# Kernel tuning notes

Measured on AMD Instinct MI355X. Metric: run time of the kernel, lower is better.

Reference implementation:

```python
import jax, jax.numpy as jnp
import numpy as np

# ---- CRF hyperparameters (init_kwargs) ----
NUM_CLASSES = 4
RADIUS = 10            # guided filter radius -> 21x21 kernel
EPS = 1e-4
THETA_GAMMA = 2.5
G_RADIUS = int(THETA_GAMMA * 4)  # gaussian layer radius = 10 -> 21x21 kernel
SPATIAL_COMPAT = 3.0
BILATERAL_COMPAT = 10.0
NUM_ITERATIONS = 5
RGB_W = np.array([0.2989, 0.5870, 0.1140], dtype=np.float32)  # tf rgb_to_grayscale


def _make_kernel(radius, theta):
    x, y = np.mgrid[-radius:radius + 1, -radius:radius + 1]
    k = np.exp(-(x ** 2 + y ** 2) / (2.0 * theta ** 2))
    k = k / k.sum()
    k[radius, radius] = 0.0  # zero out center (no self-message)
    return jnp.asarray(k, dtype=jnp.float32)

_GAUSS_K = _make_kernel(G_RADIUS, THETA_GAMMA)          # spatial gaussian kernel
_GUIDED_K = _make_kernel(RADIUS, RADIUS / 3.0)          # guided-filter gaussian kernel


def _depthwise(src, k2d, r):
    # src: [B,H,W,C], k2d: [kh,kw]; zero-padded depthwise conv (same as pad+VALID)
    c = src.shape[-1]
    kh, kw = k2d.shape
    k = jnp.broadcast_to(k2d[:, :, None, None], (kh, kw, 1, c))
    return jax.lax.conv_general_dilated(
        src, k, window_strides=(1, 1), padding=[(r, r), (r, r)],
        dimension_numbers=('NHWC', 'HWIO', 'NHWC'), feature_group_count=c)


def _gaussian(src):
    return _depthwise(src, _GAUSS_K, G_RADIUS)


def _guided(gray, p):
    # guided gaussian filter with single-channel guide `gray` [B,H,W,1]
    gf = lambda s: _depthwise(s, _GUIDED_K, RADIUS)
    mean_I = gf(gray)                       # [B,H,W,1]
    mean_p = gf(p)                          # [B,H,W,C]
    mean_Ip = gf(gray * p)
    cov_Ip = mean_Ip - mean_I * mean_p
    mean_II = gf(gray * gray)
    var_I = mean_II - mean_I * mean_I
    a = cov_Ip / (var_I + EPS)
    b = mean_p - a * mean_I
    return gf(a) * gray + gf(b)


def setup_inputs() -> dict:
    key = jax.random.key(0)
    k1, k2 = jax.random.split(key)
    unary = jax.random.normal(k1, (1, 512, 512, NUM_CLASSES), dtype=jnp.float32)
    image = jax.random.uniform(k2, (1, 512, 512, 3), dtype=jnp.float32)
    return {"unary": unary, "image": image}


def reference(unary, image):
    gray = (image @ jnp.asarray(RGB_W))[..., None]        # [B,H,W,1]
    ones = jnp.ones_like(unary)
    spatial_norm = _gaussian(ones)
    bilateral_norm = _guided(gray, ones)

    Q = jax.nn.softmax(-unary, axis=-1)
    for _ in range(NUM_ITERATIONS):
        spatial_out = _gaussian(Q) / spatial_norm
        bilateral_out = _guided(gray, Q) / bilateral_norm
        # spatial_weights = SPATIAL_COMPAT*I, bilateral_weights = BILATERAL_COMPAT*I,
        # compatibility = -I  => matmuls reduce to scalar scaling + negation
        message = SPATIAL_COMPAT * spatial_out + BILATERAL_COMPAT * bilateral_out
        pairwise = -message
        Q = jax.nn.softmax(-unary - pairwise, axis=-1)
    return Q
```

## Files before the change

kernel.cpp:

```cpp
#include <hip/hip_runtime.h>
#include <math.h>

#define W 512
#define H 512
#define NPIX (W*H)
#define RAD 10
#define KS 21
#define CRF_EPS 1e-4f

#define TX 32
#define TY 8
#define CIN (TX + 2*RAD)
#define RIN (TY + 2*RAD)
#define GX (W / TX)
#define GY (H / TY)
#define NBLK (GX*GY)
#define NVT (CIN * 4)

#define SM_BYTES 29952
#define OFF_R1 23296

#define FLAG_STRIDE 32

struct W21 { float w[KS]; };

struct Params {
    const float4* unary;
    const float*  image;
    float*  gray;
    float4* Q;
    float2* a1b1;
    float4* a_arr;
    float4* b_arr;
    float4* Qfinal;
    unsigned* flags;
    W21 wg, wu;
    float c0g, c0u;
};

__device__ __forceinline__ float4 f4(float x, float y, float z, float w_) {
    return make_float4(x, y, z, w_);
}
__device__ __forceinline__ float4 fma4(float s, float4 a, float4 acc) {
    acc.x = fmaf(s, a.x, acc.x); acc.y = fmaf(s, a.y, acc.y);
    acc.z = fmaf(s, a.z, acc.z); acc.w = fmaf(s, a.w, acc.w);
    return acc;
}
__device__ __forceinline__ int swz(int b, int N) {
    return (b & 7) * (N >> 3) + (b >> 3);
}


__device__ __forceinline__ void publish(unsigned* flags, int L, unsigned v) {
    __syncthreads();
    if (threadIdx.x == 0)
        __hip_atomic_store(flags + (size_t)L * FLAG_STRIDE, v,
                           __ATOMIC_RELEASE, __HIP_MEMORY_SCOPE_AGENT);
}

__device__ __forceinline__ void waitnb(unsigned* flags, int bx, int by, unsigned v) {
    int t = threadIdx.x;
    if (t < 15) {
        int dx = (t % 3) - 1, dy = (t / 3) - 2;
        int nx = bx + dx, ny = by + dy;
        if (((dx | dy) != 0) && (unsigned)nx < GX && (unsigned)ny < GY) {
            unsigned* f = flags + (size_t)(ny * GX + nx) * FLAG_STRIDE;
            while (__hip_atomic_load(f, __ATOMIC_ACQUIRE,
                                     __HIP_MEMORY_SCOPE_AGENT) < v)
                __builtin_amdgcn_s_sleep(4);
        }
    }
    __syncthreads();
}


__global__ __launch_bounds__(256, 5) void k_crf(Params P) {
    __shared__ __align__(16) char smem[SM_BYTES];
    float4* sQ  = (float4*)smem;
    float2* s2t = (float2*)smem;
    float2* ii0 = (float2*)smem;
    float*  sG  = (float*)(smem + OFF_R1);
    float2* ii1 = (float2*)(smem + OFF_R1);
    float4* i0  = (float4*)smem;
    float4* i1  = (float4*)(smem + 6656);
    float4* i2  = (float4*)(smem + OFF_R1);
    float4* ia  = (float4*)(smem + OFF_R1);
    float4* ib  = (float4*)smem;

    int t = threadIdx.x;
    int L = swz(blockIdx.x, NBLK);
    int bx = L & (GX - 1), by = L >> 4;
    int x0 = bx * TX, y0 = by * TY;
    int row = t >> 5, col = t & 31;
    int py = y0 + row, px = x0 + col;
    int p = py * W + px;
    int vc = t % CIN, vr0 = (t / CIN) * 2;
    int cidx = (row + RAD) * CIN + col + RAD;
    unsigned* flags = P.flags;

    float4 u = P.unary[p];
    {
        float r = P.image[3 * p], g = P.image[3 * p + 1], b = P.image[3 * p + 2];
        P.gray[p] = 0.2989f * r + 0.5870f * g + 0.1140f * b;
        float mn = fminf(fminf(u.x, u.y), fminf(u.z, u.w));
        float ex = expf(mn - u.x), ey = expf(mn - u.y);
        float ez = expf(mn - u.z), ew = expf(mn - u.w);
        float inv = 1.f / (ex + ey + ez + ew);
        P.Q[p] = f4(ex * inv, ey * inv, ez * inv, ew * inv);
    }
    float Sgx = 0.f, Sgy = 0.f, Sux = 0.f, Suy = 0.f;
    #pragma unroll
    for (int d = -RAD; d <= RAD; ++d) {
        int xx = px + d, yy = py + d;
        if (xx >= 0 && xx < W) { Sgx += P.wg.w[d + RAD]; Sux += P.wu.w[d + RAD]; }
        if (yy >= 0 && yy < H) { Sgy += P.wg.w[d + RAD]; Suy += P.wu.w[d + RAD]; }
    }
    float s3 = 3.f / (Sgx * Sgy - P.c0g);
    publish(flags, L, 1);
    waitnb(flags, bx, by, 1);

    for (int i = t; i < RIN * CIN; i += 256) {
        int r = i / CIN, c = i - r * CIN;
        int gx = x0 + c - RAD, gy = y0 + r - RAD;
        float g = 0.f;
        if ((unsigned)gx < W && (unsigned)gy < H) g = P.gray[gy * W + gx];
        sG[i] = g;
    }
    __syncthreads();
    if (t < NVT) {
        float2 acc0 = make_float2(0.f, 0.f), acc1 = acc0;
        #pragma unroll
        for (int s = 0; s < 22; ++s) {
            float g = sG[(vr0 + s) * CIN + vc];
            if (s <= 20) { float wgv = P.wu.w[s] * g; acc0.x += wgv; acc0.y = fmaf(wgv, g, acc0.y); }
            if (s >= 1)  { float wgv = P.wu.w[s-1] * g; acc1.x += wgv; acc1.y = fmaf(wgv, g, acc1.y); }
        }
        ii0[vr0 * CIN + vc] = acc0;
        ii0[(vr0 + 1) * CIN + vc] = acc1;
    }
    __syncthreads();
    float gv = sG[cidx];
    float mI, iv, ibn;
    {
        float2 A = make_float2(0.f, 0.f);
        #pragma unroll
        for (int d = 0; d < KS; ++d) {
            float2 v = ii0[row * CIN + col + d];
            A.x = fmaf(P.wu.w[d], v.x, A.x);
            A.y = fmaf(P.wu.w[d], v.y, A.y);
        }
        mI = A.x - P.c0u * gv;
        float mII = A.y - P.c0u * gv * gv;
        iv = 1.f / ((mII - mI * mI) + CRF_EPS);
        float N = Sux * Suy - P.c0u;
        float a1v = mI * (1.f - N) * iv;
        float b1v = N - a1v * mI;
        P.a1b1[p] = make_float2(a1v, b1v);
    }
    publish(flags, L, 2);
    waitnb(flags, bx, by, 2);

    for (int i = t; i < RIN * CIN; i += 256) {
        int r = i / CIN, c = i - r * CIN;
        int gx = x0 + c - RAD, gy = y0 + r - RAD;
        float2 v = make_float2(0.f, 0.f);
        if ((unsigned)gx < W && (unsigned)gy < H) v = P.a1b1[gy * W + gx];
        s2t[i] = v;
    }
    __syncthreads();
    if (t < NVT) {
        float2 acc0 = make_float2(0.f, 0.f), acc1 = acc0;
        #pragma unroll
        for (int s = 0; s < 22; ++s) {
            float2 v = s2t[(vr0 + s) * CIN + vc];
            if (s <= 20) { acc0.x = fmaf(P.wu.w[s], v.x, acc0.x); acc0.y = fmaf(P.wu.w[s], v.y, acc0.y); }
            if (s >= 1)  { acc1.x = fmaf(P.wu.w[s-1], v.x, acc1.x); acc1.y = fmaf(P.wu.w[s-1], v.y, acc1.y); }
        }
        ii1[vr0 * CIN + vc] = acc0;
        ii1[(vr0 + 1) * CIN + vc] = acc1;
    }
    __syncthreads();
    {
        float2 A = make_float2(0.f, 0.f);
        #pragma unroll
        for (int d = 0; d < KS; ++d) {
            float2 v = ii1[row * CIN + col + d];
            A.x = fmaf(P.wu.w[d], v.x, A.x);
            A.y = fmaf(P.wu.w[d], v.y, A.y);
        }
        float2 cen = s2t[cidx];
        float va = A.x - P.c0u * cen.x;
        float vb = A.y - P.c0u * cen.y;
        ibn = 10.f / (va * gv + vb);
    }

    float px_part, py_part, pz_part, pw_part;
    for (int it = 0; it < 5; ++it) {
        if (it > 0) waitnb(flags, bx, by, 2 + 2 * it);
        __syncthreads();
        for (int i = t; i < RIN * CIN; i += 256) {
            int r = i / CIN, c = i - r * CIN;
            int gx = x0 + c - RAD, gy = y0 + r - RAD;
            float4 q = f4(0.f, 0.f, 0.f, 0.f); float g = 0.f;
            if ((unsigned)gx < W && (unsigned)gy < H) {
                int pp = gy * W + gx; q = P.Q[pp]; g = P.gray[pp];
            }
            sQ[i] = q; sG[i] = g;
        }
        __syncthreads();
        float4 Qc = sQ[cidx];
        float4 a0[2], a1r[2], a2[2];
        if (t < NVT) {
            #pragma unroll
            for (int j = 0; j < 2; ++j) { a0[j] = f4(0,0,0,0); a1r[j] = a0[j]; a2[j] = a0[j]; }
            #pragma unroll
            for (int s = 0; s < 22; ++s) {
                float4 q = sQ[(vr0 + s) * CIN + vc];
                float g = sG[(vr0 + s) * CIN + vc];
                float4 gq = f4(g * q.x, g * q.y, g * q.z, g * q.w);
                if (s <= 20) {
                    a0[0]  = fma4(P.wg.w[s], q, a0[0]);
                    a1r[0] = fma4(P.wu.w[s], q, a1r[0]);
                    a2[0]  = fma4(P.wu.w[s], gq, a2[0]);
                }
                if (s >= 1) {
                    a0[1]  = fma4(P.wg.w[s-1], q, a0[1]);
                    a1r[1] = fma4(P.wu.w[s-1], q, a1r[1]);
                    a2[1]  = fma4(P.wu.w[s-1], gq, a2[1]);
                }
            }
        }
        __syncthreads();
        if (t < NVT) {
            #pragma unroll
            for (int j = 0; j < 2; ++j) {
                i0[(vr0 + j) * CIN + vc] = a0[j];
                i1[(vr0 + j) * CIN + vc] = a1r[j];
                i2[(vr0 + j) * CIN + vc] = a2[j];
            }
        }
        __syncthreads();
        {
            float4 A0 = f4(0,0,0,0), A1 = A0, A2 = A0;
            #pragma unroll
            for (int d = 0; d < KS; ++d) {
                A0 = fma4(P.wg.w[d], i0[row * CIN + col + d], A0);
                A1 = fma4(P.wu.w[d], i1[row * CIN + col + d], A1);
                A2 = fma4(P.wu.w[d], i2[row * CIN + col + d], A2);
            }
            float4 g4  = fma4(-P.c0g, Qc, A0);
            float4 m4  = fma4(-P.c0u, Qc, A1);
            float4 mi4 = fma4(-P.c0u * gv, Qc, A2);
            float4 a, b;
            a.x = (mi4.x - mI * m4.x) * iv; a.y = (mi4.y - mI * m4.y) * iv;
            a.z = (mi4.z - mI * m4.z) * iv; a.w = (mi4.w - mI * m4.w) * iv;
            b.x = m4.x - a.x * mI; b.y = m4.y - a.y * mI;
            b.z = m4.z - a.z * mI; b.w = m4.w - a.w * mI;
            px_part = fmaf(s3, g4.x, -u.x); py_part = fmaf(s3, g4.y, -u.y);
            pz_part = fmaf(s3, g4.z, -u.z); pw_part = fmaf(s3, g4.w, -u.w);
            P.a_arr[p] = a; P.b_arr[p] = b;
        }
        publish(flags, L, 3 + 2 * it);
        waitnb(flags, bx, by, 3 + 2 * it);

        for (int i = t; i < RIN * CIN; i += 256) {
            int r = i / CIN, c = i - r * CIN;
            int gx = x0 + c - RAD, gy = y0 + r - RAD;
            float4 v = f4(0.f, 0.f, 0.f, 0.f);
            if ((unsigned)gx < W && (unsigned)gy < H) v = P.a_arr[gy * W + gx];
            sQ[i] = v;
        }
        __syncthreads();
        float4 Ac = sQ[cidx];
        if (t < NVT) {
            float4 va0 = f4(0,0,0,0), va1 = va0;
            #pragma unroll
            for (int s = 0; s < 22; ++s) {
                float4 v = sQ[(vr0 + s) * CIN + vc];
                if (s <= 20) va0 = fma4(P.wu.w[s], v, va0);
                if (s >= 1)  va1 = fma4(P.wu.w[s-1], v, va1);
            }
            ia[vr0 * CIN + vc] = va0;
            ia[(vr0 + 1) * CIN + vc] = va1;
        }
        __syncthreads();
        for (int i = t; i < RIN * CIN; i += 256) {
            int r = i / CIN, c = i - r * CIN;
            int gx = x0 + c - RAD, gy = y0 + r - RAD;
            float4 v = f4(0.f, 0.f, 0.f, 0.f);
            if ((unsigned)gx < W && (unsigned)gy < H) v = P.b_arr[gy * W + gx];
            sQ[i] = v;
        }
        __syncthreads();
        float4 Bc = sQ[cidx];
        float4 vb0 = f4(0,0,0,0), vb1 = vb0;
        if (t < NVT) {
            #pragma unroll
            for (int s = 0; s < 22; ++s) {
                float4 v = sQ[(vr0 + s) * CIN + vc];
                if (s <= 20) vb0 = fma4(P.wu.w[s], v, vb0);
                if (s >= 1)  vb1 = fma4(P.wu.w[s-1], v, vb1);
            }
        }
        __syncthreads();
        if (t < NVT) {
            ib[vr0 * CIN + vc] = vb0;
            ib[(vr0 + 1) * CIN + vc] = vb1;
        }
        __syncthreads();
        {
            float4 VA = f4(0,0,0,0), VB = VA;
            #pragma unroll
            for (int d = 0; d < KS; ++d) {
                VA = fma4(P.wu.w[d], ia[row * CIN + col + d], VA);
                VB = fma4(P.wu.w[d], ib[row * CIN + col + d], VB);
            }
            float4 a4 = fma4(-P.c0u, Ac, VA);
            float4 b4 = fma4(-P.c0u, Bc, VB);
            float lx = fmaf(fmaf(a4.x, gv, b4.x), ibn, px_part);
            float ly = fmaf(fmaf(a4.y, gv, b4.y), ibn, py_part);
            float lz = fmaf(fmaf(a4.z, gv, b4.z), ibn, pz_part);
            float lw = fmaf(fmaf(a4.w, gv, b4.w), ibn, pw_part);
            float m = fmaxf(fmaxf(lx, ly), fmaxf(lz, lw));
            float ex = expf(lx - m), ey = expf(ly - m);
            float ez = expf(lz - m), ew = expf(lw - m);
            float inv = 1.f / (ex + ey + ez + ew);
            float4 qn = f4(ex * inv, ey * inv, ez * inv, ew * inv);
            if (it == 4) P.Qfinal[p] = qn;
            else         P.Q[p] = qn;
        }
        if (it < 4) publish(flags, L, 4 + 2 * it);
    }
}


__global__ __launch_bounds__(256) void fb_init(const float* __restrict__ img,
        const float4* __restrict__ unary, float* __restrict__ gray,
        float4* __restrict__ Q, float* __restrict__ Sg, float* __restrict__ Su,
        W21 wg, W21 wu) {
    int t = threadIdx.x;
    if (blockIdx.x < 2) {
        int x = blockIdx.x * 256 + t;
        float sg = 0.f, su = 0.f;
        #pragma unroll
        for (int d = -RAD; d <= RAD; ++d) {
            int xx = x + d;
            if (xx >= 0 && xx < W) { sg += wg.w[d + RAD]; su += wu.w[d + RAD]; }
        }
        Sg[x] = sg; Su[x] = su;
    }
    int b = swz(blockIdx.x, NPIX / 256);
    int p = b * 256 + t;
    float r = img[3 * p], g = img[3 * p + 1], bch = img[3 * p + 2];
    gray[p] = 0.2989f * r + 0.5870f * g + 0.1140f * bch;
    float4 u = unary[p];
    float mn = fminf(fminf(u.x, u.y), fminf(u.z, u.w));
    float ex = expf(mn - u.x), ey = expf(mn - u.y), ez = expf(mn - u.z), ew = expf(mn - u.w);
    float inv = 1.f / (ex + ey + ez + ew);
    Q[p] = f4(ex * inv, ey * inv, ez * inv, ew * inv);
}

__global__ __launch_bounds__(256, 4) void fb_s1(const float* __restrict__ gray,
        const float* __restrict__ Su, float* __restrict__ mean_I,
        float* __restrict__ inv_var, float2* __restrict__ a1b1,
        W21 wu, float c0u) {
    __shared__ float  sg[RIN][CIN];
    __shared__ float2 ii[TY][CIN];
    int L = swz(blockIdx.x, NBLK);
    int x0 = (L & (GX - 1)) * TX, y0 = (L >> 4) * TY;
    int t = threadIdx.x;
    for (int i = t; i < RIN * CIN; i += 256) {
        int r = i / CIN, c = i - r * CIN;
        int gx = x0 + c - RAD, gy = y0 + r - RAD;
        float g = 0.f;
        if ((unsigned)gx < W && (unsigned)gy < H) g = gray[gy * W + gx];
        sg[r][c] = g;
    }
    __syncthreads();
    if (t < NVT) {
        int c = t % CIN, r0 = (t / CIN) * 2;
        float2 acc0 = make_float2(0.f, 0.f), acc1 = acc0;
        #pragma unroll
        for (int s = 0; s < 22; ++s) {
            float g = sg[r0 + s][c];
            if (s <= 20) { float wgv = wu.w[s] * g; acc0.x += wgv; acc0.y = fmaf(wgv, g, acc0.y); }
            if (s >= 1)  { float wgv = wu.w[s-1] * g; acc1.x += wgv; acc1.y = fmaf(wgv, g, acc1.y); }
        }
        ii[r0][c] = acc0; ii[r0 + 1][c] = acc1;
    }
    __syncthreads();
    int row = t >> 5, col = t & 31;
    float2 A = make_float2(0.f, 0.f);
    #pragma unroll
    for (int d = 0; d < KS; ++d) {
        float2 v = ii[row][col + d];
        A.x = fmaf(wu.w[d], v.x, A.x);
        A.y = fmaf(wu.w[d], v.y, A.y);
    }
    int py = y0 + row, px = x0 + col;
    int p = py * W + px;
    float gc = sg[row + RAD][col + RAD];
    float mI = A.x - c0u * gc;
    float mII = A.y - c0u * gc * gc;
    float iv = 1.f / ((mII - mI * mI) + CRF_EPS);
    float N = Su[px] * Su[py] - c0u;
    float av = mI * (1.f - N) * iv;
    float bv = N - av * mI;
    mean_I[p] = mI; inv_var[p] = iv; a1b1[p] = make_float2(av, bv);
}

__global__ __launch_bounds__(256, 4) void fb_s2(const float2* __restrict__ a1b1,
        const float* __restrict__ gray, float* __restrict__ inv_bn,
        W21 wu, float c0u) {
    __shared__ float2 s2[RIN][CIN];
    __shared__ float2 ii[TY][CIN];
    int L = swz(blockIdx.x, NBLK);
    int x0 = (L & (GX - 1)) * TX, y0 = (L >> 4) * TY;
    int t = threadIdx.x;
    for (int i = t; i < RIN * CIN; i += 256) {
        int r = i / CIN, c = i - r * CIN;
        int gx = x0 + c - RAD, gy = y0 + r - RAD;
        float2 v = make_float2(0.f, 0.f);
        if ((unsigned)gx < W && (unsigned)gy < H) v = a1b1[gy * W + gx];
        s2[r][c] = v;
    }
    __syncthreads();
    if (t < NVT) {
        int c = t % CIN, r0 = (t / CIN) * 2;
        float2 acc0 = make_float2(0.f, 0.f), acc1 = acc0;
        #pragma unroll
        for (int s = 0; s < 22; ++s) {
            float2 v = s2[r0 + s][c];
            if (s <= 20) { acc0.x = fmaf(wu.w[s], v.x, acc0.x); acc0.y = fmaf(wu.w[s], v.y, acc0.y); }
            if (s >= 1)  { acc1.x = fmaf(wu.w[s-1], v.x, acc1.x); acc1.y = fmaf(wu.w[s-1], v.y, acc1.y); }
        }
        ii[r0][c] = acc0; ii[r0 + 1][c] = acc1;
    }
    __syncthreads();
    int row = t >> 5, col = t & 31;
    float2 A = make_float2(0.f, 0.f);
    #pragma unroll
    for (int d = 0; d < KS; ++d) {
        float2 v = ii[row][col + d];
        A.x = fmaf(wu.w[d], v.x, A.x);
        A.y = fmaf(wu.w[d], v.y, A.y);
    }
    int p = (y0 + row) * W + x0 + col;
    float2 cen = s2[row + RAD][col + RAD];
    float va = A.x - c0u * cen.x;
    float vb = A.y - c0u * cen.y;
    inv_bn[p] = 1.f / (va * gray[p] + vb);
}

__global__ __launch_bounds__(256, 4) void fb_f1(const float4* __restrict__ Q,
        const float* __restrict__ gray, const float* __restrict__ mean_I,
        const float* __restrict__ inv_var, const float* __restrict__ Sg,
        const float4* __restrict__ unary, float4* __restrict__ a_out,
        float4* __restrict__ b_out, float4* __restrict__ partial,
        W21 wg, W21 wu, float c0g, float c0u) {
    __shared__ __align__(16) char smem[23296 + 5824 + 6656];
    float4* sQ = (float4*)smem;
    float*  sG = (float*)(smem + 23296);
    float4* i2 = (float4*)(smem + 23296 + 5824);
    float4* i0 = (float4*)smem;
    float4* i1 = (float4*)(smem + 6656);
    int L = swz(blockIdx.x, NBLK);
    int x0 = (L & (GX - 1)) * TX, y0 = (L >> 4) * TY;
    int t = threadIdx.x;
    for (int i = t; i < RIN * CIN; i += 256) {
        int r = i / CIN, c = i - r * CIN;
        int gx = x0 + c - RAD, gy = y0 + r - RAD;
        float4 q = f4(0.f, 0.f, 0.f, 0.f); float g = 0.f;
        if ((unsigned)gx < W && (unsigned)gy < H) {
            int p = gy * W + gx; q = Q[p]; g = gray[p];
        }
        sQ[i] = q; sG[i] = g;
    }
    __syncthreads();
    int row = t >> 5, col = t & 31;
    int py = y0 + row, px = x0 + col;
    int p = py * W + px;
    float mI = mean_I[p], iv = inv_var[p];
    float4 u = unary[p];
    float sgx = Sg[px], sgy = Sg[py];
    float4 Qc = sQ[(row + RAD) * CIN + col + RAD];
    float  gc = sG[(row + RAD) * CIN + col + RAD];
    float4 a0[2], a1[2], a2[2];
    int vc = t % CIN, vr0 = (t / CIN) * 2;
    if (t < NVT) {
        #pragma unroll
        for (int j = 0; j < 2; ++j) { a0[j] = f4(0,0,0,0); a1[j] = a0[j]; a2[j] = a0[j]; }
        #pragma unroll
        for (int s = 0; s < 22; ++s) {
            float4 q = sQ[(vr0 + s) * CIN + vc];
            float g = sG[(vr0 + s) * CIN + vc];
            float4 gq = f4(g * q.x, g * q.y, g * q.z, g * q.w);
            if (s <= 20) {
                a0[0] = fma4(wg.w[s], q, a0[0]);
                a1[0] = fma4(wu.w[s], q, a1[0]);
                a2[0] = fma4(wu.w[s], gq, a2[0]);
            }
            if (s >= 1) {
                a0[1] = fma4(wg.w[s-1], q, a0[1]);
                a1[1] = fma4(wu.w[s-1], q, a1[1]);
                a2[1] = fma4(wu.w[s-1], gq, a2[1]);
            }
        }
    }
    __syncthreads();
    if (t < NVT) {
        #pragma unroll
        for (int j = 0; j < 2; ++j) {
            i0[(vr0 + j) * CIN + vc] = a0[j];
            i1[(vr0 + j) * CIN + vc] = a1[j];
            i2[(vr0 + j) * CIN + vc] = a2[j];
        }
    }
    __syncthreads();
    float4 A0 = f4(0,0,0,0), A1 = A0, A2 = A0;
    #pragma unroll
    for (int d = 0; d < KS; ++d) {
        A0 = fma4(wg.w[d], i0[row * CIN + col + d], A0);
        A1 = fma4(wu.w[d], i1[row * CIN + col + d], A1);
        A2 = fma4(wu.w[d], i2[row * CIN + col + d], A2);
    }
    float4 g4  = fma4(-c0g, Qc, A0);
    float4 m4  = fma4(-c0u, Qc, A1);
    float4 mi4 = fma4(-c0u * gc, Qc, A2);
    float4 a, b;
    a.x = (mi4.x - mI * m4.x) * iv; a.y = (mi4.y - mI * m4.y) * iv;
    a.z = (mi4.z - mI * m4.z) * iv; a.w = (mi4.w - mI * m4.w) * iv;
    b.x = m4.x - a.x * mI; b.y = m4.y - a.y * mI;
    b.z = m4.z - a.z * mI; b.w = m4.w - a.w * mI;
    float s3 = 3.f / (sgx * sgy - c0g);
    float4 part = f4(fmaf(s3, g4.x, -u.x), fmaf(s3, g4.y, -u.y),
                     fmaf(s3, g4.z, -u.z), fmaf(s3, g4.w, -u.w));
    a_out[p] = a; b_out[p] = b; partial[p] = part;
}

__global__ __launch_bounds__(256, 4) void fb_f2(const float4* __restrict__ A,
        const float4* __restrict__ B, const float4* __restrict__ partial,
        const float* __restrict__ gray, const float* __restrict__ inv_bn,
        float4* __restrict__ Qout, W21 wu, float c0u) {
    __shared__ __align__(16) char smem[23296 + 6656];
    float4* sT = (float4*)smem;
    float4* ia = (float4*)(smem + 23296);
    float4* ib = (float4*)smem;
    int L = swz(blockIdx.x, NBLK);
    int x0 = (L & (GX - 1)) * TX, y0 = (L >> 4) * TY;
    int t = threadIdx.x;
    int row = t >> 5, col = t & 31;
    int py = y0 + row, px = x0 + col;
    int p = py * W + px;
    int vc = t % CIN, vr0 = (t / CIN) * 2;
    float gv = gray[p];
    float ibn = 10.f * inv_bn[p];
    float4 part = partial[p];
    for (int i = t; i < RIN * CIN; i += 256) {
        int r = i / CIN, c = i - r * CIN;
        int gx = x0 + c - RAD, gy = y0 + r - RAD;
        float4 v = f4(0.f, 0.f, 0.f, 0.f);
        if ((unsigned)gx < W && (unsigned)gy < H) v = A[gy * W + gx];
        sT[i] = v;
    }
    __syncthreads();
    float4 Ac = sT[(row + RAD) * CIN + col + RAD];
    float4 va0 = f4(0,0,0,0), va1 = va0;
    if (t < NVT) {
        #pragma unroll
        for (int s = 0; s < 22; ++s) {
            float4 v = sT[(vr0 + s) * CIN + vc];
            if (s <= 20) va0 = fma4(wu.w[s], v, va0);
            if (s >= 1)  va1 = fma4(wu.w[s-1], v, va1);
        }
        ia[vr0 * CIN + vc] = va0;
        ia[(vr0 + 1) * CIN + vc] = va1;
    }
    __syncthreads();
    for (int i = t; i < RIN * CIN; i += 256) {
        int r = i / CIN, c = i - r * CIN;
        int gx = x0 + c - RAD, gy = y0 + r - RAD;
        float4 v = f4(0.f, 0.f, 0.f, 0.f);
        if ((unsigned)gx < W && (unsigned)gy < H) v = B[gy * W + gx];
        sT[i] = v;
    }
    __syncthreads();
    float4 Bc = sT[(row + RAD) * CIN + col + RAD];
    float4 vb0 = f4(0,0,0,0), vb1 = vb0;
    if (t < NVT) {
        #pragma unroll
        for (int s = 0; s < 22; ++s) {
            float4 v = sT[(vr0 + s) * CIN + vc];
            if (s <= 20) vb0 = fma4(wu.w[s], v, vb0);
            if (s >= 1)  vb1 = fma4(wu.w[s-1], v, vb1);
        }
    }
    __syncthreads();
    if (t < NVT) {
        ib[vr0 * CIN + vc] = vb0;
        ib[(vr0 + 1) * CIN + vc] = vb1;
    }
    __syncthreads();
    float4 VA = f4(0,0,0,0), VB = VA;
    #pragma unroll
    for (int d = 0; d < KS; ++d) {
        VA = fma4(wu.w[d], ia[row * CIN + col + d], VA);
        VB = fma4(wu.w[d], ib[row * CIN + col + d], VB);
    }
    float4 a4 = fma4(-c0u, Ac, VA);
    float4 b4 = fma4(-c0u, Bc, VB);
    float lx = fmaf(fmaf(a4.x, gv, b4.x), ibn, part.x);
    float ly = fmaf(fmaf(a4.y, gv, b4.y), ibn, part.y);
    float lz = fmaf(fmaf(a4.z, gv, b4.z), ibn, part.z);
    float lw = fmaf(fmaf(a4.w, gv, b4.w), ibn, part.w);
    float m = fmaxf(fmaxf(lx, ly), fmaxf(lz, lw));
    float ex = expf(lx - m), ey = expf(ly - m), ez = expf(lz - m), ew = expf(lw - m);
    float inv = 1.f / (ex + ey + ez + ew);
    Qout[p] = f4(ex * inv, ey * inv, ez * inv, ew * inv);
}


static void make_w_host(double theta, W21* w, float* c0) {
    double tmp[KS], s = 0.0;
    for (int d = -RAD; d <= RAD; ++d) {
        double v = exp(-(double)(d * d) / (2.0 * theta * theta));
        tmp[d + RAD] = v; s += v;
    }
    for (int i = 0; i < KS; ++i) w->w[i] = (float)(tmp[i] / s);
    *c0 = (float)(1.0 / (s * s));
}

extern "C" void kernel_launch(void* const* d_in, const int* in_sizes, int n_in,
                              void* d_out, int out_size, void* d_ws, size_t ws_size,
                              hipStream_t stream) {
    const float4* unary = (const float4*)d_in[0];
    const float* image = (const float*)d_in[1];
    float* wsf = (float*)d_ws;

    float*  gray    = wsf;
    float*  mean_I  = wsf + 262144;
    float*  inv_var = wsf + 524288;
    float2* a1b1    = (float2*)(wsf + 786432);
    float*  inv_bn  = wsf + 1310720;
    float*  Sg      = wsf + 1572864;
    float*  Su      = wsf + 1573376;
    float4* Q       = (float4*)(wsf + 1573888);
    float4* partial = (float4*)(wsf + 2622464);
    float4* a_arr   = (float4*)(wsf + 3671040);
    float4* b_arr   = (float4*)(wsf + 4719616);
    unsigned* flags = (unsigned*)(wsf + 262144);

    W21 wg, wu; float c0g, c0u;
    make_w_host(2.5, &wg, &c0g);
    make_w_host(10.0 / 3.0, &wu, &c0u);

    int dev = 0;
    (void)hipGetDevice(&dev);
    int coop = 0, nCU = 0, blkPerCU = 0;
    (void)hipDeviceGetAttribute(&coop, hipDeviceAttributeCooperativeLaunch, dev);
    (void)hipDeviceGetAttribute(&nCU, hipDeviceAttributeMultiprocessorCount, dev);
    (void)hipOccupancyMaxActiveBlocksPerMultiprocessor(&blkPerCU,
            (const void*)k_crf, 256, 0);
    bool useCoop = (coop != 0) && ((long)blkPerCU * nCU >= NBLK);

    hipError_t st = hipErrorUnknown;
    if (useCoop) {
        (void)hipMemsetAsync(flags, 0, (size_t)NBLK * FLAG_STRIDE * sizeof(unsigned),
                             stream);
        Params P;
        P.unary = unary; P.image = image; P.gray = gray; P.Q = Q;
        P.a1b1 = a1b1; P.a_arr = a_arr; P.b_arr = b_arr;
        P.Qfinal = (float4*)d_out; P.flags = flags;
        P.wg = wg; P.wu = wu; P.c0g = c0g; P.c0u = c0u;
        void* args[] = { &P };
        st = hipLaunchCooperativeKernel((const void*)k_crf, dim3(NBLK), dim3(256),
                                        args, 0, stream);
    }
    if (st != hipSuccess) {
        dim3 bl(256), grEl(NPIX / 256), grT(NBLK);
        fb_init<<<grEl, bl, 0, stream>>>(image, unary, gray, Q, Sg, Su, wg, wu);
        fb_s1<<<grT, bl, 0, stream>>>(gray, Su, mean_I, inv_var, a1b1, wu, c0u);
        fb_s2<<<grT, bl, 0, stream>>>(a1b1, gray, inv_bn, wu, c0u);
        for (int it = 0; it < 5; ++it) {
            fb_f1<<<grT, bl, 0, stream>>>(Q, gray, mean_I, inv_var, Sg,
                                          unary, a_arr, b_arr, partial, wg, wu, c0g, c0u);
            float4* qdst = (it == 4) ? (float4*)d_out : Q;
            fb_f2<<<grT, bl, 0, stream>>>(a_arr, b_arr, partial, gray, inv_bn, qdst,
                                          wu, c0u);
        }
    }
}
```

Before: 170.4 us.

## Register-block separable filters: 4 rows per vertical thread, 2 pixels per horizontal thread

The vertical pass now has each of 104 threads compute 4 output rows from a 24-row sliding window, where before each of 208 threads computed 2 rows from 22. The horizontal pass now has 128 threads each produce 2 adjacent pixels, reading from even/odd split shared-memory planes so each loaded value feeds both outputs. Gray is kept resident in shared memory instead of being reloaded every iteration, which enlarges the LDS footprint and lowers launch bounds from 5 to 4 waves. The aim is fewer redundant LDS reads per FMA. The cost is that only half the threads stay active in the compute phases, register pressure rises, and occupancy drops.

```diff
diff --git a/kernel.cpp b/kernel.cpp
--- a/kernel.cpp
+++ b/kernel.cpp
@@ -17,8 +17,9 @@
 #define NBLK (GX*GY)
 #define NVT (CIN * 4)
 
-#define SM_BYTES 29952
-#define OFF_R1 23296
+#define SM_BYTES 35776
+#define OFF_SG 23296
+#define OFF_R2 29120
 
 #define FLAG_STRIDE 32
 
@@ -50,7 +51,6 @@
     return (b & 7) * (N >> 3) + (b >> 3);
 }
 
-
 __device__ __forceinline__ void publish(unsigned* flags, int L, unsigned v) {
     __syncthreads();
     if (threadIdx.x == 0)
@@ -67,55 +67,70 @@
             unsigned* f = flags + (size_t)(ny * GX + nx) * FLAG_STRIDE;
             while (__hip_atomic_load(f, __ATOMIC_ACQUIRE,
                                      __HIP_MEMORY_SCOPE_AGENT) < v)
-                __builtin_amdgcn_s_sleep(4);
-        }
-    }
-    __syncthreads();
-}
-
-
-__global__ __launch_bounds__(256, 5) void k_crf(Params P) {
+                __builtin_amdgcn_s_sleep(2);
+        }
+    }
+    __syncthreads();
+}
+
+
+__global__ __launch_bounds__(256, 4) void k_crf(Params P) {
     __shared__ __align__(16) char smem[SM_BYTES];
     float4* sQ  = (float4*)smem;
     float2* s2t = (float2*)smem;
-    float2* ii0 = (float2*)smem;
-    float*  sG  = (float*)(smem + OFF_R1);
-    float2* ii1 = (float2*)(smem + OFF_R1);
-    float4* i0  = (float4*)smem;
-    float4* i1  = (float4*)(smem + 6656);
-    float4* i2  = (float4*)(smem + OFF_R1);
-    float4* ia  = (float4*)(smem + OFF_R1);
-    float4* ib  = (float4*)smem;
+    float*  sG  = (float*)(smem + OFF_SG);
+    float4* i0E = (float4*)smem;
+    float4* i1E = (float4*)(smem + 6656);
+    float4* i2E = (float4*)(smem + 13312);
+    float4* iaE = (float4*)(smem + OFF_R2);
+    float4* ibE = (float4*)smem;
+    float2* ii0E = (float2*)smem;
+    float2* ii1E = (float2*)(smem + OFF_R2);
 
     int t = threadIdx.x;
     int L = swz(blockIdx.x, NBLK);
     int bx = L & (GX - 1), by = L >> 4;
     int x0 = bx * TX, y0 = by * TY;
     int row = t >> 5, col = t & 31;
-    int py = y0 + row, px = x0 + col;
-    int p = py * W + px;
-    int vc = t % CIN, vr0 = (t / CIN) * 2;
-    int cidx = (row + RAD) * CIN + col + RAD;
+    int p = (y0 + row) * W + x0 + col;
+    int vc = t % CIN, vr4 = (t / CIN) * 4;
+    int hrow = t >> 4, hm = t & 15;
+    int c0 = 2 * hm;
+    int hpy = y0 + hrow;
+    int p0 = hpy * W + x0 + c0, p1 = p0 + 1;
+    int cidx0 = (hrow + RAD) * CIN + c0 + RAD;
+    int cidx1 = cidx0 + 1;
+    int hb = hrow * 26 + hm;
     unsigned* flags = P.flags;
 
-    float4 u = P.unary[p];
     {
         float r = P.image[3 * p], g = P.image[3 * p + 1], b = P.image[3 * p + 2];
         P.gray[p] = 0.2989f * r + 0.5870f * g + 0.1140f * b;
-        float mn = fminf(fminf(u.x, u.y), fminf(u.z, u.w));
-        float ex = expf(mn - u.x), ey = expf(mn - u.y);
-        float ez = expf(mn - u.z), ew = expf(mn - u.w);
+        float4 uu = P.unary[p];
+        float mn = fminf(fminf(uu.x, uu.y), fminf(uu.z, uu.w));
+        float ex = expf(mn - uu.x), ey = expf(mn - uu.y);
+        float ez = expf(mn - uu.z), ew = expf(mn - uu.w);
         float inv = 1.f / (ex + ey + ez + ew);
         P.Q[p] = f4(ex * inv, ey * inv, ez * inv, ew * inv);
     }
-    float Sgx = 0.f, Sgy = 0.f, Sux = 0.f, Suy = 0.f;
-    #pragma unroll
-    for (int d = -RAD; d <= RAD; ++d) {
-        int xx = px + d, yy = py + d;
-        if (xx >= 0 && xx < W) { Sgx += P.wg.w[d + RAD]; Sux += P.wu.w[d + RAD]; }
-        if (yy >= 0 && yy < H) { Sgy += P.wg.w[d + RAD]; Suy += P.wu.w[d + RAD]; }
-    }
-    float s3 = 3.f / (Sgx * Sgy - P.c0g);
+    float4 u0, u1; float s30, s31, N0, N1;
+    if (t < 128) {
+        u0 = P.unary[p0]; u1 = P.unary[p1];
+        float Sgy = 0.f, Suy = 0.f, Sgx0 = 0.f, Sux0 = 0.f, Sgx1 = 0.f, Sux1 = 0.f;
+        #pragma unroll
+        for (int d = -RAD; d <= RAD; ++d) {
+            int yy = hpy + d;
+            if ((unsigned)yy < H) { Sgy += P.wg.w[d + RAD]; Suy += P.wu.w[d + RAD]; }
+            int xa = x0 + c0 + d;
+            if ((unsigned)xa < W) { Sgx0 += P.wg.w[d + RAD]; Sux0 += P.wu.w[d + RAD]; }
+            int xb = xa + 1;
+            if ((unsigned)xb < W) { Sgx1 += P.wg.w[d + RAD]; Sux1 += P.wu.w[d + RAD]; }
+        }
+        s30 = 3.f / (Sgx0 * Sgy - P.c0g);
+        s31 = 3.f / (Sgx1 * Sgy - P.c0g);
+        N0 = Sux0 * Suy - P.c0u;
+        N1 = Sux1 * Suy - P.c0u;
+    }
     publish(flags, L, 1);
     waitnb(flags, bx, by, 1);
 
@@ -127,35 +142,61 @@
         sG[i] = g;
     }
     __syncthreads();
-    if (t < NVT) {
-        float2 acc0 = make_float2(0.f, 0.f), acc1 = acc0;
-        #pragma unroll
-        for (int s = 0; s < 22; ++s) {
-            float g = sG[(vr0 + s) * CIN + vc];
-            if (s <= 20) { float wgv = P.wu.w[s] * g; acc0.x += wgv; acc0.y = fmaf(wgv, g, acc0.y); }
-            if (s >= 1)  { float wgv = P.wu.w[s-1] * g; acc1.x += wgv; acc1.y = fmaf(wgv, g, acc1.y); }
-        }
-        ii0[vr0 * CIN + vc] = acc0;
-        ii0[(vr0 + 1) * CIN + vc] = acc1;
-    }
-    __syncthreads();
-    float gv = sG[cidx];
-    float mI, iv, ibn;
     {
-        float2 A = make_float2(0.f, 0.f);
-        #pragma unroll
-        for (int d = 0; d < KS; ++d) {
-            float2 v = ii0[row * CIN + col + d];
-            A.x = fmaf(P.wu.w[d], v.x, A.x);
-            A.y = fmaf(P.wu.w[d], v.y, A.y);
-        }
-        mI = A.x - P.c0u * gv;
-        float mII = A.y - P.c0u * gv * gv;
-        iv = 1.f / ((mII - mI * mI) + CRF_EPS);
-        float N = Sux * Suy - P.c0u;
-        float a1v = mI * (1.f - N) * iv;
-        float b1v = N - a1v * mI;
-        P.a1b1[p] = make_float2(a1v, b1v);
+        float2 A[4];
+        if (t < 104) {
+            #pragma unroll
+            for (int j = 0; j < 4; ++j) A[j] = make_float2(0.f, 0.f);
+            #pragma unroll
+            for (int s = 0; s < 24; ++s) {
+                float g = sG[(vr4 + s) * CIN + vc];
+                #pragma unroll
+                for (int j = 0; j < 4; ++j) {
+                    int d = s - j;
+                    if (d >= 0 && d <= 20) {
+                        float wgv = P.wu.w[d] * g;
+                        A[j].x += wgv; A[j].y = fmaf(wgv, g, A[j].y);
+                    }
+                }
+            }
+        }
+        __syncthreads();
+        if (t < 104) {
+            float2* pl = ii0E + (vc & 1) * 208;
+            #pragma unroll
+            for (int j = 0; j < 4; ++j) pl[(vr4 + j) * 26 + (vc >> 1)] = A[j];
+        }
+        __syncthreads();
+    }
+    float gv0 = 0.f, gv1 = 0.f, mI0, mI1, iv0, iv1, ibn0, ibn1;
+    if (t < 128) {
+        gv0 = sG[cidx0]; gv1 = sG[cidx1];
+        float2 a0 = make_float2(0.f, 0.f), a1 = a0;
+        #pragma unroll
+        for (int k = 0; k <= 10; ++k) {
+            float2 e = ii0E[hb + k], o = ii0E[208 + hb + k];
+            float we = P.wu.w[2 * k];
+            a0.x = fmaf(we, e.x, a0.x); a0.y = fmaf(we, e.y, a0.y);
+            a1.x = fmaf(we, o.x, a1.x); a1.y = fmaf(we, o.y, a1.y);
+            if (k < 10) {
+                float wo = P.wu.w[2 * k + 1];
+                a0.x = fmaf(wo, o.x, a0.x); a0.y = fmaf(wo, o.y, a0.y);
+            }
+            if (k > 0) {
+                float wp = P.wu.w[2 * k - 1];
+                a1.x = fmaf(wp, e.x, a1.x); a1.y = fmaf(wp, e.y, a1.y);
+            }
+        }
+        mI0 = a0.x - P.c0u * gv0;
+        float mII0 = a0.y - P.c0u * gv0 * gv0;
+        iv0 = 1.f / ((mII0 - mI0 * mI0) + CRF_EPS);
+        float av0 = mI0 * (1.f - N0) * iv0;
+        P.a1b1[p0] = make_float2(av0, N0 - av0 * mI0);
+        mI1 = a1.x - P.c0u * gv1;
+        float mII1 = a1.y - P.c0u * gv1 * gv1;
+        iv1 = 1.f / ((mII1 - mI1 * mI1) + CRF_EPS);
+        float av1 = mI1 * (1.f - N1) * iv1;
+        P.a1b1[p1] = make_float2(av1, N1 - av1 * mI1);
     }
     publish(flags, L, 2);
     waitnb(flags, bx, by, 2);
@@ -168,97 +209,157 @@
         s2t[i] = v;
     }
     __syncthreads();
-    if (t < NVT) {
-        float2 acc0 = make_float2(0.f, 0.f), acc1 = acc0;
-        #pragma unroll
-        for (int s = 0; s < 22; ++s) {
-            float2 v = s2t[(vr0 + s) * CIN + vc];
-            if (s <= 20) { acc0.x = fmaf(P.wu.w[s], v.x, acc0.x); acc0.y = fmaf(P.wu.w[s], v.y, acc0.y); }
-            if (s >= 1)  { acc1.x = fmaf(P.wu.w[s-1], v.x, acc1.x); acc1.y = fmaf(P.wu.w[s-1], v.y, acc1.y); }
-        }
-        ii1[vr0 * CIN + vc] = acc0;
-        ii1[(vr0 + 1) * CIN + vc] = acc1;
-    }
-    __syncthreads();
     {
-        float2 A = make_float2(0.f, 0.f);
-        #pragma unroll
-        for (int d = 0; d < KS; ++d) {
-            float2 v = ii1[row * CIN + col + d];
-            A.x = fmaf(P.wu.w[d], v.x, A.x);
-            A.y = fmaf(P.wu.w[d], v.y, A.y);
-        }
-        float2 cen = s2t[cidx];
-        float va = A.x - P.c0u * cen.x;
-        float vb = A.y - P.c0u * cen.y;
-        ibn = 10.f / (va * gv + vb);
-    }
-
-    float px_part, py_part, pz_part, pw_part;
+        float2 A[4];
+        if (t < 104) {
+            #pragma unroll
+            for (int j = 0; j < 4; ++j) A[j] = make_float2(0.f, 0.f);
+            #pragma unroll
+            for (int s = 0; s < 24; ++s) {
+                float2 v = s2t[(vr4 + s) * CIN + vc];
+                #pragma unroll
+                for (int j = 0; j < 4; ++j) {
+                    int d = s - j;
+                    if (d >= 0 && d <= 20) {
+                        float w_ = P.wu.w[d];
+                        A[j].x = fmaf(w_, v.x, A[j].x);
+                        A[j].y = fmaf(w_, v.y, A[j].y);
+                    }
+                }
+            }
+        }
+        __syncthreads();
+        if (t < 104) {
+            float2* pl = ii1E + (vc & 1) * 208;
+            #pragma unroll
+            for (int j = 0; j < 4; ++j) pl[(vr4 + j) * 26 + (vc >> 1)] = A[j];
+        }
+        __syncthreads();
+    }
+    if (t < 128) {
+        float2 a0 = make_float2(0.f, 0.f), a1 = a0;
+        #pragma unroll
+        for (int k = 0; k <= 10; ++k) {
+            float2 e = ii1E[hb + k], o = ii1E[208 + hb + k];
+            float we = P.wu.w[2 * k];
+            a0.x = fmaf(we, e.x, a0.x); a0.y = fmaf(we, e.y, a0.y);
+            a1.x = fmaf(we, o.x, a1.x); a1.y = fmaf(we, o.y, a1.y);
+            if (k < 10) {
+                float wo = P.wu.w[2 * k + 1];
+                a0.x = fmaf(wo, o.x, a0.x); a0.y = fmaf(wo, o.y, a0.y);
+            }
+            if (k > 0) {
+                float wp = P.wu.w[2 * k - 1];
+                a1.x = fmaf(wp, e.x, a1.x); a1.y = fmaf(wp, e.y, a1.y);
+            }
+        }
+        float2 cen0 = s2t[cidx0], cen1 = s2t[cidx1];
+        float va0 = a0.x - P.c0u * cen0.x, vb0 = a0.y - P.c0u * cen0.y;
+        ibn0 = 10.f / (va0 * gv0 + vb0);
+        float va1 = a1.x - P.c0u * cen1.x, vb1 = a1.y - P.c0u * cen1.y;
+        ibn1 = 10.f / (va1 * gv1 + vb1);
+    }
+
+    float4 part0, part1;
     for (int it = 0; it < 5; ++it) {
         if (it > 0) waitnb(flags, bx, by, 2 + 2 * it);
         __syncthreads();
         for (int i = t; i < RIN * CIN; i += 256) {
             int r = i / CIN, c = i - r * CIN;
             int gx = x0 + c - RAD, gy = y0 + r - RAD;
-            float4 q = f4(0.f, 0.f, 0.f, 0.f); float g = 0.f;
-            if ((unsigned)gx < W && (unsigned)gy < H) {
-                int pp = gy * W + gx; q = P.Q[pp]; g = P.gray[pp];
-            }
-            sQ[i] = q; sG[i] = g;
+            float4 q = f4(0.f, 0.f, 0.f, 0.f);
+            if ((unsigned)gx < W && (unsigned)gy < H) q = P.Q[gy * W + gx];
+            sQ[i] = q;
         }
         __syncthreads();
-        float4 Qc = sQ[cidx];
-        float4 a0[2], a1r[2], a2[2];
-        if (t < NVT) {
-            #pragma unroll
-            for (int j = 0; j < 2; ++j) { a0[j] = f4(0,0,0,0); a1r[j] = a0[j]; a2[j] = a0[j]; }
-            #pragma unroll
-            for (int s = 0; s < 22; ++s) {
-                float4 q = sQ[(vr0 + s) * CIN + vc];
-                float g = sG[(vr0 + s) * CIN + vc];
-                float4 gq = f4(g * q.x, g * q.y, g * q.z, g * q.w);
-                if (s <= 20) {
-                    a0[0]  = fma4(P.wg.w[s], q, a0[0]);
-                    a1r[0] = fma4(P.wu.w[s], q, a1r[0]);
-                    a2[0]  = fma4(P.wu.w[s], gq, a2[0]);
-                }
-                if (s >= 1) {
-                    a0[1]  = fma4(P.wg.w[s-1], q, a0[1]);
-                    a1r[1] = fma4(P.wu.w[s-1], q, a1r[1]);
-                    a2[1]  = fma4(P.wu.w[s-1], gq, a2[1]);
-                }
-            }
-        }
-        __syncthreads();
-        if (t < NVT) {
-            #pragma unroll
-            for (int j = 0; j < 2; ++j) {
-                i0[(vr0 + j) * CIN + vc] = a0[j];
-                i1[(vr0 + j) * CIN + vc] = a1r[j];
-                i2[(vr0 + j) * CIN + vc] = a2[j];
-            }
-        }
-        __syncthreads();
+        float4 Qc0, Qc1;
+        if (t < 128) { Qc0 = sQ[cidx0]; Qc1 = sQ[cidx1]; }
         {
-            float4 A0 = f4(0,0,0,0), A1 = A0, A2 = A0;
-            #pragma unroll
-            for (int d = 0; d < KS; ++d) {
-                A0 = fma4(P.wg.w[d], i0[row * CIN + col + d], A0);
-                A1 = fma4(P.wu.w[d], i1[row * CIN + col + d], A1);
-                A2 = fma4(P.wu.w[d], i2[row * CIN + col + d], A2);
-            }
-            float4 g4  = fma4(-P.c0g, Qc, A0);
-            float4 m4  = fma4(-P.c0u, Qc, A1);
-            float4 mi4 = fma4(-P.c0u * gv, Qc, A2);
-            float4 a, b;
-            a.x = (mi4.x - mI * m4.x) * iv; a.y = (mi4.y - mI * m4.y) * iv;
-            a.z = (mi4.z - mI * m4.z) * iv; a.w = (mi4.w - mI * m4.w) * iv;
-            b.x = m4.x - a.x * mI; b.y = m4.y - a.y * mI;
-            b.z = m4.z - a.z * mI; b.w = m4.w - a.w * mI;
-            px_part = fmaf(s3, g4.x, -u.x); py_part = fmaf(s3, g4.y, -u.y);
-            pz_part = fmaf(s3, g4.z, -u.z); pw_part = fmaf(s3, g4.w, -u.w);
-            P.a_arr[p] = a; P.b_arr[p] = b;
+            float4 A0[4], A1[4], A2[4];
+            if (t < 104) {
+                #pragma unroll
+                for (int j = 0; j < 4; ++j) {
+                    A0[j] = f4(0,0,0,0); A1[j] = A0[j]; A2[j] = A0[j];
+                }
+                #pragma unroll
+                for (int s = 0; s < 24; ++s) {
+                    float4 q = sQ[(vr4 + s) * CIN + vc];
+                    float g = sG[(vr4 + s) * CIN + vc];
+                    float4 gq = f4(g * q.x, g * q.y, g * q.z, g * q.w);
+                    #pragma unroll
+                    for (int j = 0; j < 4; ++j) {
+                        int d = s - j;
+                        if (d >= 0 && d <= 20) {
+                            A0[j] = fma4(P.wg.w[d], q, A0[j]);
+                            A1[j] = fma4(P.wu.w[d], q, A1[j]);
+                            A2[j] = fma4(P.wu.w[d], gq, A2[j]);
+                        }
+                    }
+                }
+            }
+            __syncthreads();
+            if (t < 104) {
+                int pb = (vc & 1) * 208, ci = vc >> 1;
+                #pragma unroll
+                for (int j = 0; j < 4; ++j) {
+                    int rw = (vr4 + j) * 26 + ci;
+                    i0E[pb + rw] = A0[j];
+                    i1E[pb + rw] = A1[j];
+                    i2E[pb + rw] = A2[j];
+                }
+            }
+            __syncthreads();
+        }
+        if (t < 128) {
+            float4 G0 = f4(0,0,0,0), G1 = G0, M0 = G0, M1 = G0, X0 = G0, X1 = G0;
+            #pragma unroll
+            for (int k = 0; k <= 10; ++k) {
+                float4 e0 = i0E[hb + k], o0 = i0E[208 + hb + k];
+                float4 e1 = i1E[hb + k], o1 = i1E[208 + hb + k];
+                float4 e2 = i2E[hb + k], o2 = i2E[208 + hb + k];
+                float wge = P.wg.w[2 * k], wue = P.wu.w[2 * k];
+                G0 = fma4(wge, e0, G0);  G1 = fma4(wge, o0, G1);
+                M0 = fma4(wue, e1, M0);  M1 = fma4(wue, o1, M1);
+                X0 = fma4(wue, e2, X0);  X1 = fma4(wue, o2, X1);
+                if (k < 10) {
+                    float wgo = P.wg.w[2 * k + 1], wuo = P.wu.w[2 * k + 1];
+                    G0 = fma4(wgo, o0, G0);
+                    M0 = fma4(wuo, o1, M0);
+                    X0 = fma4(wuo, o2, X0);
+                }
+                if (k > 0) {
+                    float wgp = P.wg.w[2 * k - 1], wup = P.wu.w[2 * k - 1];
+                    G1 = fma4(wgp, e0, G1);
+                    M1 = fma4(wup, e1, M1);
+                    X1 = fma4(wup, e2, X1);
+                }
+            }
+            {
+                float4 g4  = fma4(-P.c0g, Qc0, G0);
+                float4 m4  = fma4(-P.c0u, Qc0, M0);
+                float4 mi4 = fma4(-P.c0u * gv0, Qc0, X0);
+                float4 a, b;
+                a.x = (mi4.x - mI0 * m4.x) * iv0; a.y = (mi4.y - mI0 * m4.y) * iv0;
+                a.z = (mi4.z - mI0 * m4.z) * iv0; a.w = (mi4.w - mI0 * m4.w) * iv0;
+                b.x = m4.x - a.x * mI0; b.y = m4.y - a.y * mI0;
+                b.z = m4.z - a.z * mI0; b.w = m4.w - a.w * mI0;
+                part0 = f4(fmaf(s30, g4.x, -u0.x), fmaf(s30, g4.y, -u0.y),
+                           fmaf(s30, g4.z, -u0.z), fmaf(s30, g4.w, -u0.w));
+                P.a_arr[p0] = a; P.b_arr[p0] = b;
+            }
+            {
+                float4 g4  = fma4(-P.c0g, Qc1, G1);
+                float4 m4  = fma4(-P.c0u, Qc1, M1);
+                float4 mi4 = fma4(-P.c0u * gv1, Qc1, X1);
+                float4 a, b;
+                a.x = (mi4.x - mI1 * m4.x) * iv1; a.y = (mi4.y - mI1 * m4.y) * iv1;
+                a.z = (mi4.z - mI1 * m4.z) * iv1; a.w = (mi4.w - mI1 * m4.w) * iv1;
+                b.x = m4.x - a.x * mI1; b.y = m4.y - a.y * mI1;
+                b.z = m4.z - a.z * mI1; b.w = m4.w - a.w * mI1;
+                part1 = f4(fmaf(s31, g4.x, -u1.x), fmaf(s31, g4.y, -u1.y),
+                           fmaf(s31, g4.z, -u1.z), fmaf(s31, g4.w, -u1.w));
+                P.a_arr[p1] = a; P.b_arr[p1] = b;
+            }
         }
         publish(flags, L, 3 + 2 * it);
         waitnb(flags, bx, by, 3 + 2 * it);
@@ -271,17 +372,24 @@
             sQ[i] = v;
         }
         __syncthreads();
-        float4 Ac = sQ[cidx];
-        if (t < NVT) {
-            float4 va0 = f4(0,0,0,0), va1 = va0;
-            #pragma unroll
-            for (int s = 0; s < 22; ++s) {
-                float4 v = sQ[(vr0 + s) * CIN + vc];
-                if (s <= 20) va0 = fma4(P.wu.w[s], v, va0);
-                if (s >= 1)  va1 = fma4(P.wu.w[s-1], v, va1);
-            }
-            ia[vr0 * CIN + vc] = va0;
-            ia[(vr0 + 1) * CIN + vc] = va1;
+        float4 Ac0, Ac1;
+        if (t < 128) { Ac0 = sQ[cidx0]; Ac1 = sQ[cidx1]; }
+        if (t < 104) {
+            float4 VA[4];
+            #pragma unroll
+            for (int j = 0; j < 4; ++j) VA[j] = f4(0,0,0,0);
+            #pragma unroll
+            for (int s = 0; s < 24; ++s) {
+                float4 v = sQ[(vr4 + s) * CIN + vc];
+                #pragma unroll
+                for (int j = 0; j < 4; ++j) {
+                    int d = s - j;
+                    if (d >= 0 && d <= 20) VA[j] = fma4(P.wu.w[d], v, VA[j]);
+                }
+            }
+            int pb = (vc & 1) * 208, ci = vc >> 1;
+            #pragma unroll
+            for (int j = 0; j < 4; ++j) iaE[pb + (vr4 + j) * 26 + ci] = VA[j];
         }
         __syncthreads();
         for (int i = t; i < RIN * CIN; i += 256) {
@@ -292,42 +400,79 @@
             sQ[i] = v;
         }
         __syncthreads();
-        float4 Bc = sQ[cidx];
-        float4 vb0 = f4(0,0,0,0), vb1 = vb0;
-        if (t < NVT) {
-            #pragma unroll
-            for (int s = 0; s < 22; ++s) {
-                float4 v = sQ[(vr0 + s) * CIN + vc];
-                if (s <= 20) vb0 = fma4(P.wu.w[s], v, vb0);
-                if (s >= 1)  vb1 = fma4(P.wu.w[s-1], v, vb1);
-            }
-        }
-        __syncthreads();
-        if (t < NVT) {
-            ib[vr0 * CIN + vc] = vb0;
-            ib[(vr0 + 1) * CIN + vc] = vb1;
-        }
-        __syncthreads();
+        float4 Bc0, Bc1;
+        if (t < 128) { Bc0 = sQ[cidx0]; Bc1 = sQ[cidx1]; }
         {
-            float4 VA = f4(0,0,0,0), VB = VA;
-            #pragma unroll
-            for (int d = 0; d < KS; ++d) {
-                VA = fma4(P.wu.w[d], ia[row * CIN + col + d], VA);
-                VB = fma4(P.wu.w[d], ib[row * CIN + col + d], VB);
-            }
-            float4 a4 = fma4(-P.c0u, Ac, VA);
-            float4 b4 = fma4(-P.c0u, Bc, VB);
-            float lx = fmaf(fmaf(a4.x, gv, b4.x), ibn, px_part);
-            float ly = fmaf(fmaf(a4.y, gv, b4.y), ibn, py_part);
-            float lz = fmaf(fmaf(a4.z, gv, b4.z), ibn, pz_part);
-            float lw = fmaf(fmaf(a4.w, gv, b4.w), ibn, pw_part);
-            float m = fmaxf(fmaxf(lx, ly), fmaxf(lz, lw));
-            float ex = expf(lx - m), ey = expf(ly - m);
-            float ez = expf(lz - m), ew = expf(lw - m);
-            float inv = 1.f / (ex + ey + ez + ew);
-            float4 qn = f4(ex * inv, ey * inv, ez * inv, ew * inv);
-            if (it == 4) P.Qfinal[p] = qn;
-            else         P.Q[p] = qn;
+            float4 VB[4];
+            if (t < 104) {
+                #pragma unroll
+                for (int j = 0; j < 4; ++j) VB[j] = f4(0,0,0,0);
+                #pragma unroll
+                for (int s = 0; s < 24; ++s) {
+                    float4 v = sQ[(vr4 + s) * CIN + vc];
+                    #pragma unroll
+                    for (int j = 0; j < 4; ++j) {
+                        int d = s - j;
+                        if (d >= 0 && d <= 20) VB[j] = fma4(P.wu.w[d], v, VB[j]);
+                    }
+                }
+            }
+            __syncthreads();
+            if (t < 104) {
+                int pb = (vc & 1) * 208, ci = vc >> 1;
+                #pragma unroll
+                for (int j = 0; j < 4; ++j) ibE[pb + (vr4 + j) * 26 + ci] = VB[j];
+            }
+            __syncthreads();
+        }
+        if (t < 128) {
+            float4 VA0 = f4(0,0,0,0), VA1 = VA0, VB0 = VA0, VB1 = VA0;
+            #pragma unroll
+            for (int k = 0; k <= 10; ++k) {
+                float4 ea = iaE[hb + k], oa = iaE[208 + hb + k];
+                float4 eb = ibE[hb + k], ob = ibE[208 + hb + k];
+                float wue = P.wu.w[2 * k];
+                VA0 = fma4(wue, ea, VA0);  VA1 = fma4(wue, oa, VA1);
+                VB0 = fma4(wue, eb, VB0);  VB1 = fma4(wue, ob, VB1);
+                if (k < 10) {
+                    float wuo = P.wu.w[2 * k + 1];
+                    VA0 = fma4(wuo, oa, VA0);
+                    VB0 = fma4(wuo, ob, VB0);
+                }
+                if (k > 0) {
+                    float wup = P.wu.w[2 * k - 1];
+                    VA1 = fma4(wup, ea, VA1);
+                    VB1 = fma4(wup, eb, VB1);
+                }
+            }
+            {
+                float4 a4 = fma4(-P.c0u, Ac0, VA0);
+                float4 b4 = fma4(-P.c0u, Bc0, VB0);
+                float lx = fmaf(fmaf(a4.x, gv0, b4.x), ibn0, part0.x);
+                float ly = fmaf(fmaf(a4.y, gv0, b4.y), ibn0, part0.y);
+                float lz = fmaf(fmaf(a4.z, gv0, b4.z), ibn0, part0.z);
+                float lw = fmaf(fmaf(a4.w, gv0, b4.w), ibn0, part0.w);
+                float m = fmaxf(fmaxf(lx, ly), fmaxf(lz, lw));
+                float ex = expf(lx - m), ey = expf(ly - m);
+                float ez = expf(lz - m), ew = expf(lw - m);
+                float inv = 1.f / (ex + ey + ez + ew);
+                float4 qn = f4(ex * inv, ey * inv, ez * inv, ew * inv);
+                if (it == 4) P.Qfinal[p0] = qn; else P.Q[p0] = qn;
+            }
+            {
+                float4 a4 = fma4(-P.c0u, Ac1, VA1);
+                float4 b4 = fma4(-P.c0u, Bc1, VB1);
+                float lx = fmaf(fmaf(a4.x, gv1, b4.x), ibn1, part1.x);
+                float ly = fmaf(fmaf(a4.y, gv1, b4.y), ibn1, part1.y);
+                float lz = fmaf(fmaf(a4.z, gv1, b4.z), ibn1, part1.z);
+                float lw = fmaf(fmaf(a4.w, gv1, b4.w), ibn1, part1.w);
+                float m = fmaxf(fmaxf(lx, ly), fmaxf(lz, lw));
+                float ex = expf(lx - m), ey = expf(ly - m);
+                float ez = expf(lz - m), ew = expf(lw - m);
+                float inv = 1.f / (ex + ey + ez + ew);
+                float4 qn = f4(ex * inv, ey * inv, ez * inv, ew * inv);
+                if (it == 4) P.Qfinal[p1] = qn; else P.Q[p1] = qn;
+            }
         }
         if (it < 4) publish(flags, L, 4 + 2 * it);
     }
```

Result: no change. 170.2 us (-0.1%).
